# Kernel tuning notes

Measured on AMD Instinct MI355X. Metric: run time of the kernel, lower is better.

## Reference

```python
import jax, jax.numpy as jnp
import numpy as np

H = 16  # head_num


def setup_inputs() -> dict:
    key = jax.random.key(0)
    ks = jax.random.split(key, 16)
    B, N, D, DR = 4, 512, 1024, 128
    dk = D // H
    nrm = lambda i, shp, sc=1.0: jax.random.normal(ks[i], shp, jnp.float32) * sc
    inp = {
        "q": nrm(0, (B, N, D)),
        "k": nrm(1, (B, N, D)),
        "v": nrm(2, (B, N, D)),
        "r_k": nrm(3, (B, N, N, DR), 0.1),
        "r_v": nrm(4, (B, N, N, DR), 0.1),
        # learned params (Linear stored as [in, out] so y = x @ W + b)
        "Wq": nrm(5, (D, D), 1.0 / np.sqrt(D)), "bq": jnp.zeros((D,), jnp.float32),
        "Wk": nrm(6, (D, D), 1.0 / np.sqrt(D)), "bk": jnp.zeros((D,), jnp.float32),
        "Wv": nrm(7, (D, D), 1.0 / np.sqrt(D)), "bv": jnp.zeros((D,), jnp.float32),
        "Wrk": nrm(8, (DR, dk), 1.0 / np.sqrt(DR)), "brk": jnp.zeros((dk,), jnp.float32),
        "Wrv": nrm(9, (DR, dk), 1.0 / np.sqrt(DR)), "brv": jnp.zeros((dk,), jnp.float32),
        "Wo": nrm(10, (D, D), 1.0 / np.sqrt(D)), "bo": jnp.zeros((D,), jnp.float32),
    }
    return inp


def reference(q, k, v, r_k, r_v, Wq, bq, Wk, bk, Wv, bv, Wrk, brk, Wrv, brv, Wo, bo):
    B, N, D = q.shape
    dk = D // H
    scale = 1.0 / np.sqrt(dk).astype(np.float32)
    # relation projections ('concat' mode, rel_share=False): [B,N,N,d_rel] -> [B,N,N,d_k]
    rk = r_k @ Wrk + brk
    rv = r_v @ Wrv + brv

    def heads(x, W, b):  # [B,N,D] -> [B,H,N,dk]
        return (x @ W + b).reshape(B, N, H, dk).transpose(0, 2, 1, 3)

    qh = heads(q, Wq, bq)
    kh = heads(k, Wk, bk)
    vh = heads(v, Wv, bv)
    # score_1: standard scaled dot-product; score_2: relation bias per (query m, key n)
    score = jnp.einsum('bhmd,bhnd->bhmn', qh, kh) * scale \
          + jnp.einsum('bhmd,bmnd->bhmn', qh, rk)
    att = jax.nn.softmax(score, axis=-1)  # [B,H,N,N]
    # value_1: standard AV; value_2: relation-value combination
    val = jnp.einsum('bhmn,bhnd->bhmd', att, vh) \
        + jnp.einsum('bhmn,bmnd->bhmd', att, rv)
    out = val.transpose(0, 2, 1, 3).reshape(B, N, D) @ Wo + bo
    return out
```

## Files before the change

### kernel.cpp

```cpp
#include <hip/hip_runtime.h>
#include <hip/hip_bf16.h>
#include <hip/hip_fp16.h>
#include <stdint.h>


typedef __attribute__((ext_vector_type(4))) float f32x4;
typedef __attribute__((ext_vector_type(8))) short s16x8;

#define MFMA16(A, B, C) __builtin_amdgcn_mfma_f32_16x16x32_bf16(A, B, C, 0, 0, 0)

__device__ __forceinline__ uint16_t f2bf(float x) {
  uint32_t u = __float_as_uint(x);
  u += 0x7fffu + ((u >> 16) & 1u);
  return (uint16_t)(u >> 16);
}
__device__ __forceinline__ float bf2f(uint16_t u) {
  return __uint_as_float((uint32_t)u << 16);
}
__device__ __forceinline__ uint16_t f2h(float x) {
  __half h = __float2half_rn(x);
  return *reinterpret_cast<uint16_t*>(&h);
}
__device__ __forceinline__ float h2f(uint16_t u) {
  __half h = *reinterpret_cast<__half*>(&u);
  return __half2float(h);
}

__device__ __forceinline__ s16x8 pack8(float4 a, float4 b) {
  s16x8 r;
  r[0] = (short)f2bf(a.x); r[1] = (short)f2bf(a.y); r[2] = (short)f2bf(a.z); r[3] = (short)f2bf(a.w);
  r[4] = (short)f2bf(b.x); r[5] = (short)f2bf(b.y); r[6] = (short)f2bf(b.z); r[7] = (short)f2bf(b.w);
  return r;
}

__device__ __forceinline__ void gll16(const void* g, void* l) {
  __builtin_amdgcn_global_load_lds(
      (const __attribute__((address_space(1))) uint32_t*)(g),
      (__attribute__((address_space(3))) uint32_t*)(l), 16, 0, 0);
}

__global__ __launch_bounds__(256) void k_prep(
    const float* __restrict__ Wq, const float* __restrict__ Wk,
    const float* __restrict__ Wv, const float* __restrict__ Wo,
    const float* __restrict__ Wrk, const float* __restrict__ Wrv,
    uint16_t* __restrict__ WqT, uint16_t* __restrict__ WkT,
    uint16_t* __restrict__ WvT, uint16_t* __restrict__ WoT,
    uint16_t* __restrict__ WrkB, uint16_t* __restrict__ WrvT) {
  int z = blockIdx.y;
  int t = threadIdx.x;
  if (z == 4) {
    if (blockIdx.x == 0) {
      for (int i = t; i < 128 * 64; i += 256) WrkB[i] = f2bf(Wrk[i]);
      for (int i = t; i < 64 * 128; i += 256) {
        int d = i >> 7, r = i & 127;
        WrvT[i] = f2bf(Wrv[r * 64 + d]);
      }
    }
    return;
  }
  const float* W = (z == 0) ? Wq : (z == 1) ? Wk : (z == 2) ? Wv : Wo;
  uint16_t* O = (z == 0) ? WqT : (z == 1) ? WkT : (z == 2) ? WvT : WoT;
  int tk = (blockIdx.x >> 4) * 64;
  int tn = (blockIdx.x & 15) * 64;
  __shared__ float tile[64][65];
  {
    int kk = t >> 2, c0 = (t & 3) * 16;
    const float* src = W + (size_t)(tk + kk) * 1024 + tn + c0;
#pragma unroll
    for (int i = 0; i < 16; i += 4) {
      float4 v = *(const float4*)(src + i);
      tile[kk][c0 + i + 0] = v.x; tile[kk][c0 + i + 1] = v.y;
      tile[kk][c0 + i + 2] = v.z; tile[kk][c0 + i + 3] = v.w;
    }
  }
  __syncthreads();
  {
    int n_loc = t >> 2;
    int n = tn + n_loc;
#pragma unroll
    for (int cc = 0; cc < 2; ++cc) {
      int c = (t & 3) * 2 + cc;
      int csrc = c ^ (n & 7);
      s16x8 pk;
#pragma unroll
      for (int j = 0; j < 8; ++j) pk[j] = (short)f2bf(tile[csrc * 8 + j][n_loc]);
      *reinterpret_cast<s16x8*>(O + (size_t)n * 1024 + tk + c * 8) = pk;
    }
  }
}

__global__ __launch_bounds__(256) void k_projqkv(
    const float* __restrict__ Xq, const float* __restrict__ Xk,
    const float* __restrict__ Xv, const uint16_t* __restrict__ WTbase,
    const float* __restrict__ bq, const float* __restrict__ bk,
    const float* __restrict__ bv, uint16_t* __restrict__ outbase) {
  int mode = blockIdx.z;
  const float* X = (mode == 0) ? Xq : (mode == 1) ? Xk : Xv;
  const float* bias = (mode == 0) ? bq : (mode == 1) ? bk : bv;
  const uint16_t* WT = WTbase + (size_t)mode * (1u << 20);
  uint16_t* out = outbase + (size_t)mode * (2u << 20);

  __shared__ alignas(16) uint16_t As[128 * 64];
  __shared__ alignas(16) uint16_t Bs[128 * 64];
  int t = threadIdx.x, lane = t & 63, w = t >> 6, lr = lane & 15, lg = lane >> 4;
  int m0 = blockIdx.x * 128, n0 = blockIdx.y * 128;
  int wm = (w >> 1) * 64, wn = (w & 1) * 64;
  f32x4 acc[4][4];
#pragma unroll
  for (int i = 0; i < 4; ++i)
#pragma unroll
    for (int j = 0; j < 4; ++j) acc[i][j] = (f32x4){0.f, 0.f, 0.f, 0.f};
  int srow = t >> 1, sh = t & 1;
  for (int ko = 0; ko < 16; ++ko) {
    __syncthreads();
    {
#pragma unroll
      for (int i = 0; i < 4; ++i) {
        int u = i * 256 + t;
        int row = u >> 3, c2 = u & 7;
        gll16(WT + (size_t)(n0 + row) * 1024 + ko * 64 + c2 * 8, (char*)Bs + u * 16);
      }
      const float* src = X + (size_t)(m0 + srow) * 1024 + ko * 64 + sh * 32;
#pragma unroll
      for (int c = 0; c < 4; ++c) {
        float4 v0 = *(const float4*)(src + c * 8);
        float4 v1 = *(const float4*)(src + c * 8 + 4);
        s16x8 pk = pack8(v0, v1);
        *reinterpret_cast<s16x8*>((char*)As + srow * 128 +
                                  ((((sh * 4 + c) * 16)) ^ ((srow & 7) << 4))) = pk;
      }
    }
    __syncthreads();
#pragma unroll
    for (int kk = 0; kk < 2; ++kk) {
      s16x8 af[4], bf[4];
#pragma unroll
      for (int mt = 0; mt < 4; ++mt) {
        int row = wm + mt * 16 + lr;
        af[mt] = *(const s16x8*)((const char*)As + row * 128 +
                                 (((kk * 32 + lg * 8) * 2) ^ ((row & 7) << 4)));
      }
#pragma unroll
      for (int nt = 0; nt < 4; ++nt) {
        int row = wn + nt * 16 + lr;
        bf[nt] = *(const s16x8*)((const char*)Bs + row * 128 +
                                 (((kk * 32 + lg * 8) * 2) ^ ((row & 7) << 4)));
      }
#pragma unroll
      for (int mt = 0; mt < 4; ++mt)
#pragma unroll
        for (int nt = 0; nt < 4; ++nt)
          acc[mt][nt] = MFMA16(af[mt], bf[nt], acc[mt][nt]);
    }
  }
  float sc = (mode == 1) ? 0.125f : 1.0f;
#pragma unroll
  for (int mt = 0; mt < 4; ++mt) {
#pragma unroll
    for (int nt = 0; nt < 4; ++nt) {
      int col = n0 + wn + nt * 16 + lr;
      float bcol = bias[col];
      if (mode != 2) {
#pragma unroll
        for (int r = 0; r < 4; ++r) {
          int row = m0 + wm + mt * 16 + lg * 4 + r;
          out[(size_t)row * 1024 + col] = f2bf((acc[mt][nt][r] + bcol) * sc);
        }
      } else {
        int row0 = m0 + wm + mt * 16 + lg * 4;
        int b = row0 >> 9, n = row0 & 511;
        int h = col >> 6, d = col & 63;
        ushort4 pk;
        pk.x = f2bf(acc[mt][nt][0] + bcol);
        pk.y = f2bf(acc[mt][nt][1] + bcol);
        pk.z = f2bf(acc[mt][nt][2] + bcol);
        pk.w = f2bf(acc[mt][nt][3] + bcol);
        *reinterpret_cast<ushort4*>(out + ((size_t)(b * 16 + h) * 64 + d) * 512 + n) = pk;
      }
    }
  }
}

__global__ __launch_bounds__(256) void k_qt(
    const uint16_t* __restrict__ qh, const uint16_t* __restrict__ WrkB,
    uint16_t* __restrict__ qt) {
  int t = threadIdx.x, lane = t & 63, w = t >> 6, lr = lane & 15, lg = lane >> 4;
  int row0 = blockIdx.x * 64 + w * 16;
  f32x4 acc[8];
#pragma unroll
  for (int i = 0; i < 8; ++i) acc[i] = (f32x4){0.f, 0.f, 0.f, 0.f};
  s16x8 af[2];
#pragma unroll
  for (int kk = 0; kk < 2; ++kk)
    af[kk] = *(const s16x8*)(qh + (size_t)(row0 + lr) * 64 + kk * 32 + lg * 8);
#pragma unroll
  for (int rt = 0; rt < 8; ++rt) {
#pragma unroll
    for (int kk = 0; kk < 2; ++kk) {
      s16x8 bf = *(const s16x8*)(WrkB + (size_t)(rt * 16 + lr) * 64 + kk * 32 + lg * 8);
      acc[rt] = MFMA16(af[kk], bf, acc[rt]);
    }
  }
#pragma unroll
  for (int rt = 0; rt < 8; ++rt)
#pragma unroll
    for (int r = 0; r < 4; ++r)
      qt[(size_t)(row0 + lg * 4 + r) * 128 + rt * 16 + lr] = f2bf(acc[rt][r]);
}

__global__ __launch_bounds__(256) void k_score1(
    const uint16_t* __restrict__ qh, const uint16_t* __restrict__ kh,
    uint16_t* __restrict__ S1) {
  __shared__ alignas(16) uint16_t As[128 * 64];
  __shared__ alignas(16) uint16_t Bs[128 * 64];
  int t = threadIdx.x, lane = t & 63, w = t >> 6, lr = lane & 15, lg = lane >> 4;
  int mt = blockIdx.x >> 2, nt = blockIdx.x & 3, h = blockIdx.y, b = blockIdx.z;
  int m0 = mt * 128, n0 = nt * 128;
  const char* qg = (const char*)(qh + (size_t)(b * 512 + m0) * 1024 + h * 64);
  const char* kg = (const char*)(kh + (size_t)(b * 512 + n0) * 1024 + h * 64);
#pragma unroll
  for (int i = 0; i < 4; ++i) {
    int u = i * 256 + t;
    int row = u >> 3;
    int cs = (u & 7) ^ (row & 7);
    gll16(qg + (size_t)row * 2048 + cs * 16, (char*)As + u * 16);
    gll16(kg + (size_t)row * 2048 + cs * 16, (char*)Bs + u * 16);
  }
  __syncthreads();
  int wm = (w >> 1) * 64, wn = (w & 1) * 64;
  f32x4 acc[4][4];
#pragma unroll
  for (int i = 0; i < 4; ++i)
#pragma unroll
    for (int j = 0; j < 4; ++j) acc[i][j] = (f32x4){0.f, 0.f, 0.f, 0.f};
#pragma unroll
  for (int kk = 0; kk < 2; ++kk) {
    s16x8 af[4], bf[4];
#pragma unroll
    for (int mtt = 0; mtt < 4; ++mtt) {
      int row = wm + mtt * 16 + lr;
      af[mtt] = *(const s16x8*)((const char*)As + row * 128 +
                                (((kk * 4 + lg) ^ (row & 7)) * 16));
    }
#pragma unroll
    for (int ntt = 0; ntt < 4; ++ntt) {
      int row = wn + ntt * 16 + lr;
      bf[ntt] = *(const s16x8*)((const char*)Bs + row * 128 +
                                (((kk * 4 + lg) ^ (row & 7)) * 16));
    }
#pragma unroll
    for (int mtt = 0; mtt < 4; ++mtt)
#pragma unroll
      for (int ntt = 0; ntt < 4; ++ntt)
        acc[mtt][ntt] = MFMA16(bf[ntt], af[mtt], acc[mtt][ntt]);
  }
  int hsw = (h & 7) << 3;
#pragma unroll
  for (int mtt = 0; mtt < 4; ++mtt) {
#pragma unroll
    for (int ntt = 0; ntt < 4; ++ntt) {
      int m = b * 512 + m0 + wm + mtt * 16 + lr;
      int nsw = (n0 + wn + ntt * 16 + lg * 4) ^ hsw;
      ushort4 u4;
      u4.x = f2h(acc[mtt][ntt][0]); u4.y = f2h(acc[mtt][ntt][1]);
      u4.z = f2h(acc[mtt][ntt][2]); u4.w = f2h(acc[mtt][ntt][3]);
      *(ushort4*)(S1 + (size_t)m * 8192 + h * 512 + nsw) = u4;
    }
  }
}

#define RKSTEP(s)                                                              \
  {                                                                            \
    asm volatile("s_waitcnt vmcnt(%0)" :: "i"(((s) < 31) ? 2 : 0) : "memory"); \
    const char* bp_ = wpriv + ((s) & 1) * 2048 + lr * 128;                     \
    float4 v0_ = *(const float4*)(bp_ + (((lg * 2 + 0) ^ (lr & 7)) * 16));     \
    float4 v1_ = *(const float4*)(bp_ + (((lg * 2 + 1) ^ (lr & 7)) * 16));     \
    acc[(s) >> 2] = MFMA16(aqt[(s) & 3], pack8(v0_, v1_), acc[(s) >> 2]);      \
    if ((s) + 2 < 32) {                                                        \
      const int s2_ = (s) + 2;                                                 \
      const char* src_ = rkb + (size_t)((s2_ >> 2) * 64 + w * 16 + r_lo) * 512 \
                         + (s2_ & 3) * 128 + c16s * 16;                        \
      char* dst_ = wpriv + (s2_ & 1) * 2048 + lane * 16;                       \
      gll16(src_, dst_);                                                       \
      gll16(src_ + 8 * 512, dst_ + 1024);                                      \
    }                                                                          \
  }

#define RVI(c)                                                                 \
  { _Pragma("unroll")                                                          \
    for (int i_ = 0; i_ < 2; ++i_) {                                           \
      int u_ = i_ * 64 + lane;                                                 \
      gll16(rvb + (size_t)(((c) >> 1) * 32 + (u_ >> 2)) * 512 + w * 128 +      \
                ((c) & 1) * 64 + (u_ & 3) * 16,                                \
            wpriv + ((c) & 1) * 2048 + u_ * 16);                               \
    } }

#define RVC(c, accv)                                                           \
  {                                                                            \
    s16x8 a_ = *(const s16x8*)((const char*)att_lds + lr * 1024 +              \
        (((uint32_t)(((c) >> 1) * 64 + lg * 16)) ^ ((uint32_t)(lr & 7) << 4)));\
    const float* vb_ = (const float*)(wpriv + ((c) & 1) * 2048);               \
    s16x8 bf_;                                                                 \
    _Pragma("unroll")                                                          \
    for (int i = 0; i < 8; ++i) bf_[i] = (short)f2bf(vb_[(lg * 8 + i) * 16 + lr]); \
    accv = MFMA16(a_, bf_, accv);                                              \
  }

__global__ __launch_bounds__(256, 4) void k_s2v2(
    const uint16_t* __restrict__ qt, const float* __restrict__ rk,
    const float* __restrict__ rv, uint16_t* SATT,
    const uint16_t* __restrict__ WrvT, const float* __restrict__ brv,
    uint16_t* __restrict__ V2) {
  int bm = blockIdx.x;
  int t = threadIdx.x, lane = t & 63, w = t >> 6, lr = lane & 15, lg = lane >> 4;
  __shared__ alignas(16) char stream_lds[16384];
  __shared__ alignas(16) uint16_t att_lds[16 * 512];
  __shared__ alignas(16) uint16_t arv_lds[16 * 128];
  __shared__ float red[2][16][4];
  char* wpriv = stream_lds + w * 4096;
  const int r_lo = lane >> 3;
  const int c16s = (lane & 7) ^ r_lo;

  s16x8 aqt[4];
#pragma unroll
  for (int kk = 0; kk < 4; ++kk)
    aqt[kk] = *(const s16x8*)(qt + ((size_t)bm * 16 + lr) * 128 + kk * 32 + lg * 8);
  const char* s1g = (const char*)(SATT + (size_t)bm * 8192);
#pragma unroll
  for (int i = 0; i < 4; ++i)
    gll16(s1g + i * 4096 + t * 16, (char*)att_lds + i * 4096 + t * 16);
  asm volatile("s_waitcnt vmcnt(0)" ::: "memory");

  const char* rkb = (const char*)(rk + (size_t)bm * 65536);
#pragma unroll
  for (int s2 = 0; s2 < 2; ++s2) {
    const char* src_ = rkb + (size_t)(w * 16 + r_lo) * 512 + s2 * 128 + c16s * 16;
    char* dst_ = wpriv + s2 * 2048 + lane * 16;
    gll16(src_, dst_);
    gll16(src_ + 8 * 512, dst_ + 1024);
  }

  f32x4 acc[8];
#pragma unroll
  for (int j = 0; j < 8; ++j) acc[j] = (f32x4){0.f, 0.f, 0.f, 0.f};

  RKSTEP(0)  RKSTEP(1)  RKSTEP(2)  RKSTEP(3)  RKSTEP(4)  RKSTEP(5)  RKSTEP(6)  RKSTEP(7)
  RKSTEP(8)  RKSTEP(9)  RKSTEP(10) RKSTEP(11) RKSTEP(12) RKSTEP(13) RKSTEP(14) RKSTEP(15)
  RKSTEP(16) RKSTEP(17) RKSTEP(18) RKSTEP(19) RKSTEP(20) RKSTEP(21) RKSTEP(22) RKSTEP(23)
  RKSTEP(24) RKSTEP(25) RKSTEP(26) RKSTEP(27) RKSTEP(28) RKSTEP(29) RKSTEP(30) RKSTEP(31)

  const char* rvb = (const char*)(rv + (size_t)bm * 65536);
  RVI(0) RVI(1)
  __syncthreads();

#pragma unroll
  for (int idx = 0; idx < 8; ++idx) {
#pragma unroll
    for (int r = 0; r < 4; ++r) {
      int h = lg * 4 + r;
      int n = idx * 64 + w * 16 + lr;
      uint16_t s1v = *(const uint16_t*)((const char*)att_lds + h * 1024 +
                     (((uint32_t)n * 2) ^ ((uint32_t)(h & 7) << 4)));
      acc[idx][r] += h2f(s1v);
    }
  }

  float mrow[4], inv[4];
#pragma unroll
  for (int r = 0; r < 4; ++r) {
    float mx = acc[0][r];
#pragma unroll
    for (int j = 1; j < 8; ++j) mx = fmaxf(mx, acc[j][r]);
#pragma unroll
    for (int off = 1; off < 16; off <<= 1) mx = fmaxf(mx, __shfl_xor(mx, off, 64));
    mrow[r] = mx;
  }
  if (lr == 0) {
#pragma unroll
    for (int r = 0; r < 4; ++r) red[0][lg * 4 + r][w] = mrow[r];
  }
  __syncthreads();
#pragma unroll
  for (int r = 0; r < 4; ++r) {
    const float* p = red[0][lg * 4 + r];
    mrow[r] = fmaxf(fmaxf(p[0], p[1]), fmaxf(p[2], p[3]));
  }
#pragma unroll
  for (int r = 0; r < 4; ++r) {
    float s = 0.f;
#pragma unroll
    for (int j = 0; j < 8; ++j) {
      float pj = __expf(acc[j][r] - mrow[r]);
      acc[j][r] = pj;
      s += pj;
    }
#pragma unroll
    for (int off = 1; off < 16; off <<= 1) s += __shfl_xor(s, off, 64);
    inv[r] = s;
  }
  if (lr == 0) {
#pragma unroll
    for (int r = 0; r < 4; ++r) red[1][lg * 4 + r][w] = inv[r];
  }
  __syncthreads();
#pragma unroll
  for (int r = 0; r < 4; ++r) {
    const float* p = red[1][lg * 4 + r];
    inv[r] = 1.f / (p[0] + p[1] + p[2] + p[3]);
  }
#pragma unroll
  for (int r = 0; r < 4; ++r) {
    int h = lg * 4 + r;
#pragma unroll
    for (int idx = 0; idx < 8; ++idx) {
      int n = idx * 64 + w * 16 + lr;
      uint32_t off = (uint32_t)h * 1024 + (((uint32_t)n * 2) ^ ((uint32_t)(h & 7) << 4));
      *(uint16_t*)((char*)att_lds + off) = f2bf(acc[idx][r] * inv[r]);
    }
  }
  __syncthreads();

  f32x4 arv0 = (f32x4){0.f, 0.f, 0.f, 0.f}, arv1 = arv0;
#pragma unroll 1
  for (int cp = 0; cp < 14; ++cp) {
    asm volatile("s_waitcnt vmcnt(2)" ::: "memory");
    RVC(2 * cp, arv0)
    RVI(2 * cp + 2)
    asm volatile("s_waitcnt vmcnt(2)" ::: "memory");
    RVC(2 * cp + 1, arv1)
    RVI(2 * cp + 3)
  }
  asm volatile("s_waitcnt vmcnt(2)" ::: "memory");
  RVC(28, arv0)
  RVI(30)
  asm volatile("s_waitcnt vmcnt(2)" ::: "memory");
  RVC(29, arv1)
  RVI(31)
  asm volatile("s_waitcnt vmcnt(2)" ::: "memory");
  RVC(30, arv0)
  asm volatile("s_waitcnt vmcnt(0)" ::: "memory");
  RVC(31, arv1)

#pragma unroll
  for (int r = 0; r < 4; ++r) {
    int h = lg * 4 + r;
    uint32_t rc0 = (uint32_t)(w * 32 + lr) * 2;
    uint32_t rc1 = (uint32_t)(w * 32 + 16 + lr) * 2;
    *(uint16_t*)((char*)arv_lds + h * 256 + (rc0 ^ ((uint32_t)(h & 7) << 4))) = f2bf(arv0[r]);
    *(uint16_t*)((char*)arv_lds + h * 256 + (rc1 ^ ((uint32_t)(h & 7) << 4))) = f2bf(arv1[r]);
  }
  __syncthreads();
  f32x4 vacc = (f32x4){0.f, 0.f, 0.f, 0.f};
#pragma unroll
  for (int kk = 0; kk < 4; ++kk) {
    uint32_t rb = (uint32_t)(kk * 32 + lg * 8) * 2;
    s16x8 a = *(const s16x8*)((const char*)arv_lds + lr * 256 +
                              (rb ^ ((uint32_t)(lr & 7) << 4)));
    s16x8 bfw = *(const s16x8*)(WrvT + (size_t)(w * 16 + lr) * 128 + kk * 32 + lg * 8);
    vacc = MFMA16(a, bfw, vacc);
  }
  float bias = brv[w * 16 + lr];
#pragma unroll
  for (int r = 0; r < 4; ++r)
    V2[(size_t)bm * 1024 + (lg * 4 + r) * 64 + w * 16 + lr] = f2bf(vacc[r] + bias);

#pragma unroll
  for (int i = 0; i < 4; ++i) {
    s16x8 vv = *(const s16x8*)((const char*)att_lds + i * 4096 + t * 16);
    *(s16x8*)((char*)SATT + (size_t)bm * 16384 + i * 4096 + t * 16) = vv;
  }
}

__global__ __launch_bounds__(256) void k_val1(
    const uint16_t* __restrict__ vhT, const uint16_t* __restrict__ ATT,
    const uint16_t* __restrict__ V2, uint16_t* __restrict__ VALB) {
  int t = threadIdx.x, lane = t & 63, w = t >> 6, lr = lane & 15, lg = lane >> 4;
  int mt = blockIdx.x >> 1, dh = blockIdx.x & 1, h = blockIdx.y, b = blockIdx.z;
  int mb = mt * 64 + w * 16;
  const uint16_t* vrow = vhT + ((size_t)((b * 16 + h) * 64) + dh * 32 + lr) * 512 + lg * 8;
  const uint16_t* arow = ATT + (size_t)(b * 512 + mb + lr) * 8192 + h * 512;
  f32x4 acc[2];
#pragma unroll
  for (int j = 0; j < 2; ++j) acc[j] = (f32x4){0.f, 0.f, 0.f, 0.f};
#pragma unroll 4
  for (int kk = 0; kk < 16; ++kk) {
    int nsw = (kk * 32 + lg * 8) ^ ((h & 7) << 3);
    s16x8 a0 = *(const s16x8*)(arow + nsw);
#pragma unroll
    for (int dt = 0; dt < 2; ++dt) {
      s16x8 vf = *(const s16x8*)(vrow + (size_t)dt * 16 * 512 + kk * 32);
      acc[dt] = MFMA16(vf, a0, acc[dt]);
    }
  }
#pragma unroll
  for (int dt = 0; dt < 2; ++dt) {
    size_t adr = (size_t)(b * 512 + mb + lr) * 1024 + h * 64 + dh * 32 + dt * 16 + lg * 4;
    ushort4 v2v = *(const ushort4*)(V2 + adr);
    ushort4 o;
    o.x = f2bf(acc[dt][0] + bf2f(v2v.x));
    o.y = f2bf(acc[dt][1] + bf2f(v2v.y));
    o.z = f2bf(acc[dt][2] + bf2f(v2v.z));
    o.w = f2bf(acc[dt][3] + bf2f(v2v.w));
    *(ushort4*)(VALB + adr) = o;
  }
}

__global__ __launch_bounds__(256) void k_out(
    const uint16_t* __restrict__ A, const uint16_t* __restrict__ WT,
    const float* __restrict__ bias, float* __restrict__ out) {
  __shared__ alignas(16) uint16_t As[128 * 64];
  __shared__ alignas(16) uint16_t Bs[128 * 64];
  int t = threadIdx.x, lane = t & 63, w = t >> 6, lr = lane & 15, lg = lane >> 4;
  int m0 = blockIdx.x * 128, n0 = blockIdx.y * 128;
  int wm = (w >> 1) * 64, wn = (w & 1) * 64;
  f32x4 acc[4][4];
#pragma unroll
  for (int i = 0; i < 4; ++i)
#pragma unroll
    for (int j = 0; j < 4; ++j) acc[i][j] = (f32x4){0.f, 0.f, 0.f, 0.f};
  int srow = t >> 1, sh = t & 1;
  for (int ko = 0; ko < 16; ++ko) {
    __syncthreads();
    {
#pragma unroll
      for (int i = 0; i < 4; ++i) {
        int u = i * 256 + t;
        int row = u >> 3, c2 = u & 7;
        gll16(WT + (size_t)(n0 + row) * 1024 + ko * 64 + c2 * 8, (char*)Bs + u * 16);
      }
      const uint16_t* asrc = A + (size_t)(m0 + srow) * 1024 + ko * 64 + sh * 32;
#pragma unroll
      for (int c = 0; c < 4; ++c) {
        s16x8 va = *(const s16x8*)(asrc + c * 8);
        *reinterpret_cast<s16x8*>((char*)As + srow * 128 +
                                  ((((sh * 4 + c) * 16)) ^ ((srow & 7) << 4))) = va;
      }
    }
    __syncthreads();
#pragma unroll
    for (int kk = 0; kk < 2; ++kk) {
      s16x8 af[4], bf[4];
#pragma unroll
      for (int mt = 0; mt < 4; ++mt) {
        int row = wm + mt * 16 + lr;
        af[mt] = *(const s16x8*)((const char*)As + row * 128 +
                                 (((kk * 32 + lg * 8) * 2) ^ ((row & 7) << 4)));
      }
#pragma unroll
      for (int nt = 0; nt < 4; ++nt) {
        int row = wn + nt * 16 + lr;
        bf[nt] = *(const s16x8*)((const char*)Bs + row * 128 +
                                 (((kk * 32 + lg * 8) * 2) ^ ((row & 7) << 4)));
      }
#pragma unroll
      for (int mt = 0; mt < 4; ++mt)
#pragma unroll
        for (int nt = 0; nt < 4; ++nt)
          acc[mt][nt] = MFMA16(af[mt], bf[nt], acc[mt][nt]);
    }
  }
#pragma unroll
  for (int mt = 0; mt < 4; ++mt) {
#pragma unroll
    for (int nt = 0; nt < 4; ++nt) {
      int col = n0 + wn + nt * 16 + lr;
      float bcol = bias[col];
#pragma unroll
      for (int r = 0; r < 4; ++r) {
        int row = m0 + wm + mt * 16 + lg * 4 + r;
        out[(size_t)row * 1024 + col] = acc[mt][nt][r] + bcol;
      }
    }
  }
}

extern "C" void kernel_launch(void* const* d_in, const int* in_sizes, int n_in,
                              void* d_out, int out_size, void* d_ws, size_t ws_size,
                              hipStream_t stream) {
  const float* q   = (const float*)d_in[0];
  const float* k_  = (const float*)d_in[1];
  const float* v   = (const float*)d_in[2];
  const float* r_k = (const float*)d_in[3];
  const float* r_v = (const float*)d_in[4];
  const float* Wq  = (const float*)d_in[5];
  const float* bq  = (const float*)d_in[6];
  const float* Wk  = (const float*)d_in[7];
  const float* bk  = (const float*)d_in[8];
  const float* Wv  = (const float*)d_in[9];
  const float* bv  = (const float*)d_in[10];
  const float* Wrk = (const float*)d_in[11];
  const float* Wrv = (const float*)d_in[13];
  const float* brv = (const float*)d_in[14];
  const float* Wo  = (const float*)d_in[15];
  const float* bo  = (const float*)d_in[16];
  (void)in_sizes; (void)n_in; (void)out_size;

  char* ws = (char*)d_ws;
  uint16_t* WqT  = (uint16_t*)(ws + (size_t)(0));
  uint16_t* WkT  = (uint16_t*)(ws + (size_t)(2u << 20));
  uint16_t* WvT  = (uint16_t*)(ws + (size_t)(4u << 20));
  uint16_t* WoT  = (uint16_t*)(ws + (size_t)(6u << 20));
  uint16_t* WrkB = (uint16_t*)(ws + (size_t)(8u << 20));
  uint16_t* WrvT = (uint16_t*)(ws + (size_t)(8u << 20) + (64u << 10));
  uint16_t* QH   = (uint16_t*)(ws + (size_t)(16u << 20));
  uint16_t* KH   = (uint16_t*)(ws + (size_t)(20u << 20));
  uint16_t* VHT  = (uint16_t*)(ws + (size_t)(24u << 20));
  uint16_t* QT   = (uint16_t*)(ws + (size_t)(28u << 20));
  uint16_t* VALB = (uint16_t*)(ws + (size_t)(36u << 20));
  uint16_t* V2   = (uint16_t*)(ws + (size_t)(16u << 20));
  uint16_t* SATT = (uint16_t*)(ws + (size_t)(40u << 20));
  if (ws_size < (size_t)(74u << 20)) return;

  dim3 blk(256, 1, 1);
  k_prep<<<dim3(256, 5, 1), blk, 0, stream>>>(Wq, Wk, Wv, Wo, Wrk, Wrv,
                                              WqT, WkT, WvT, WoT, WrkB, WrvT);
  k_projqkv<<<dim3(16, 8, 3), blk, 0, stream>>>(q, k_, v, WqT, bq, bk, bv, QH);
  k_qt<<<dim3(512, 1, 1), blk, 0, stream>>>(QH, WrkB, QT);
  k_score1<<<dim3(16, 16, 4), blk, 0, stream>>>(QH, KH, SATT);
  k_s2v2<<<dim3(2048, 1, 1), blk, 0, stream>>>(QT, r_k, r_v, SATT, WrvT, brv, V2);
  k_val1<<<dim3(16, 16, 4), blk, 0, stream>>>(VHT, SATT, V2, VALB);
  k_out<<<dim3(16, 8, 1), blk, 0, stream>>>(VALB, WoT, bo, (float*)d_out);
}
```

Before: 382.4 us.

## Merge qt and score1 launches, use packed bf16 converts, overlap S1 load

Folds the small qt projection kernel into the score1 launch as extra blocks along the y grid dimension, removing one kernel launch and letting both run concurrently. Replaces scalar float-to-bf16 rounding with the hardware v_cvt_pk_bf16_f32 instruction in pack8 and the rv conversion path. In k_s2v2, the S1 attention-row load is issued after the first rk prefetches, with adjusted vmcnt waits, so it overlaps the rk stream instead of stalling up front. The barrier is moved before the rv loads. The packed convert may round slightly differently from the manual routine.

```diff
diff --git a/kernel.cpp b/kernel.cpp
--- a/kernel.cpp
+++ b/kernel.cpp
@@ -26,11 +26,19 @@
   return __half2float(h);
 }
 
+__device__ __forceinline__ uint32_t cvtpk(float lo, float hi) {
+  uint32_t r;
+  asm("v_cvt_pk_bf16_f32 %0, %1, %2" : "=v"(r) : "v"(lo), "v"(hi));
+  return r;
+}
+
 __device__ __forceinline__ s16x8 pack8(float4 a, float4 b) {
-  s16x8 r;
-  r[0] = (short)f2bf(a.x); r[1] = (short)f2bf(a.y); r[2] = (short)f2bf(a.z); r[3] = (short)f2bf(a.w);
-  r[4] = (short)f2bf(b.x); r[5] = (short)f2bf(b.y); r[6] = (short)f2bf(b.z); r[7] = (short)f2bf(b.w);
-  return r;
+  union { uint32_t u[4]; s16x8 v; } r;
+  r.u[0] = cvtpk(a.x, a.y);
+  r.u[1] = cvtpk(a.z, a.w);
+  r.u[2] = cvtpk(b.x, b.y);
+  r.u[3] = cvtpk(b.z, b.w);
+  return r.v;
 }
 
 __device__ __forceinline__ void gll16(const void* g, void* l) {
@@ -181,40 +189,43 @@
   }
 }
 
-__global__ __launch_bounds__(256) void k_qt(
-    const uint16_t* __restrict__ qh, const uint16_t* __restrict__ WrkB,
+__global__ __launch_bounds__(256) void k_score1qt(
+    const uint16_t* __restrict__ qh, const uint16_t* __restrict__ kh,
+    const uint16_t* __restrict__ WrkB, uint16_t* __restrict__ S1,
     uint16_t* __restrict__ qt) {
-  int t = threadIdx.x, lane = t & 63, w = t >> 6, lr = lane & 15, lg = lane >> 4;
-  int row0 = blockIdx.x * 64 + w * 16;
-  f32x4 acc[8];
-#pragma unroll
-  for (int i = 0; i < 8; ++i) acc[i] = (f32x4){0.f, 0.f, 0.f, 0.f};
-  s16x8 af[2];
-#pragma unroll
-  for (int kk = 0; kk < 2; ++kk)
-    af[kk] = *(const s16x8*)(qh + (size_t)(row0 + lr) * 64 + kk * 32 + lg * 8);
-#pragma unroll
-  for (int rt = 0; rt < 8; ++rt) {
-#pragma unroll
-    for (int kk = 0; kk < 2; ++kk) {
-      s16x8 bf = *(const s16x8*)(WrkB + (size_t)(rt * 16 + lr) * 64 + kk * 32 + lg * 8);
-      acc[rt] = MFMA16(af[kk], bf, acc[rt]);
-    }
-  }
-#pragma unroll
-  for (int rt = 0; rt < 8; ++rt)
-#pragma unroll
-    for (int r = 0; r < 4; ++r)
-      qt[(size_t)(row0 + lg * 4 + r) * 128 + rt * 16 + lr] = f2bf(acc[rt][r]);
-}
-
-__global__ __launch_bounds__(256) void k_score1(
-    const uint16_t* __restrict__ qh, const uint16_t* __restrict__ kh,
-    uint16_t* __restrict__ S1) {
   __shared__ alignas(16) uint16_t As[128 * 64];
   __shared__ alignas(16) uint16_t Bs[128 * 64];
   int t = threadIdx.x, lane = t & 63, w = t >> 6, lr = lane & 15, lg = lane >> 4;
-  int mt = blockIdx.x >> 2, nt = blockIdx.x & 3, h = blockIdx.y, b = blockIdx.z;
+  int b = blockIdx.z;
+  if (blockIdx.y >= 16) {
+    int slot = (blockIdx.y - 16) * 64 + b * 16 + blockIdx.x;
+#pragma unroll
+    for (int it = 0; it < 2; ++it) {
+      int row0 = slot * 128 + it * 64 + w * 16;
+      f32x4 acc[8];
+#pragma unroll
+      for (int i = 0; i < 8; ++i) acc[i] = (f32x4){0.f, 0.f, 0.f, 0.f};
+      s16x8 af[2];
+#pragma unroll
+      for (int kk = 0; kk < 2; ++kk)
+        af[kk] = *(const s16x8*)(qh + (size_t)(row0 + lr) * 64 + kk * 32 + lg * 8);
+#pragma unroll
+      for (int rt = 0; rt < 8; ++rt) {
+#pragma unroll
+        for (int kk = 0; kk < 2; ++kk) {
+          s16x8 bf = *(const s16x8*)(WrkB + (size_t)(rt * 16 + lr) * 64 + kk * 32 + lg * 8);
+          acc[rt] = MFMA16(af[kk], bf, acc[rt]);
+        }
+      }
+#pragma unroll
+      for (int rt = 0; rt < 8; ++rt)
+#pragma unroll
+        for (int r = 0; r < 4; ++r)
+          qt[(size_t)(row0 + lg * 4 + r) * 128 + rt * 16 + lr] = f2bf(acc[rt][r]);
+    }
+    return;
+  }
+  int mt = blockIdx.x >> 2, nt = blockIdx.x & 3, h = blockIdx.y;
   int m0 = mt * 128, n0 = nt * 128;
   const char* qg = (const char*)(qh + (size_t)(b * 512 + m0) * 1024 + h * 64);
   const char* kg = (const char*)(kh + (size_t)(b * 512 + n0) * 1024 + h * 64);
@@ -271,7 +282,8 @@
 
 #define RKSTEP(s)                                                              \
   {                                                                            \
-    asm volatile("s_waitcnt vmcnt(%0)" :: "i"(((s) < 31) ? 2 : 0) : "memory"); \
+    asm volatile("s_waitcnt vmcnt(%0)" ::                                      \
+                 "i"(((s) < 2) ? 6 : (((s) < 31) ? 2 : 0)) : "memory");        \
     const char* bp_ = wpriv + ((s) & 1) * 2048 + lr * 128;                     \
     float4 v0_ = *(const float4*)(bp_ + (((lg * 2 + 0) ^ (lr & 7)) * 16));     \
     float4 v1_ = *(const float4*)(bp_ + (((lg * 2 + 1) ^ (lr & 7)) * 16));     \
@@ -300,10 +312,12 @@
     s16x8 a_ = *(const s16x8*)((const char*)att_lds + lr * 1024 +              \
         (((uint32_t)(((c) >> 1) * 64 + lg * 16)) ^ ((uint32_t)(lr & 7) << 4)));\
     const float* vb_ = (const float*)(wpriv + ((c) & 1) * 2048);               \
-    s16x8 bf_;                                                                 \
+    union { uint32_t u[4]; s16x8 v; } bb_;                                     \
     _Pragma("unroll")                                                          \
-    for (int i = 0; i < 8; ++i) bf_[i] = (short)f2bf(vb_[(lg * 8 + i) * 16 + lr]); \
-    accv = MFMA16(a_, bf_, accv);                                              \
+    for (int i = 0; i < 4; ++i)                                                \
+      bb_.u[i] = cvtpk(vb_[(lg * 8 + 2 * i) * 16 + lr],                        \
+                       vb_[(lg * 8 + 2 * i + 1) * 16 + lr]);                   \
+    accv = MFMA16(a_, bb_.v, accv);                                            \
   }
 
 __global__ __launch_bounds__(256, 4) void k_s2v2(
@@ -325,11 +339,6 @@
 #pragma unroll
   for (int kk = 0; kk < 4; ++kk)
     aqt[kk] = *(const s16x8*)(qt + ((size_t)bm * 16 + lr) * 128 + kk * 32 + lg * 8);
-  const char* s1g = (const char*)(SATT + (size_t)bm * 8192);
-#pragma unroll
-  for (int i = 0; i < 4; ++i)
-    gll16(s1g + i * 4096 + t * 16, (char*)att_lds + i * 4096 + t * 16);
-  asm volatile("s_waitcnt vmcnt(0)" ::: "memory");
 
   const char* rkb = (const char*)(rk + (size_t)bm * 65536);
 #pragma unroll
@@ -339,6 +348,10 @@
     gll16(src_, dst_);
     gll16(src_ + 8 * 512, dst_ + 1024);
   }
+  const char* s1g = (const char*)(SATT + (size_t)bm * 8192);
+#pragma unroll
+  for (int i = 0; i < 4; ++i)
+    gll16(s1g + i * 4096 + t * 16, (char*)att_lds + i * 4096 + t * 16);
 
   f32x4 acc[8];
 #pragma unroll
@@ -349,9 +362,10 @@
   RKSTEP(16) RKSTEP(17) RKSTEP(18) RKSTEP(19) RKSTEP(20) RKSTEP(21) RKSTEP(22) RKSTEP(23)
   RKSTEP(24) RKSTEP(25) RKSTEP(26) RKSTEP(27) RKSTEP(28) RKSTEP(29) RKSTEP(30) RKSTEP(31)
 
+  __syncthreads();
+
   const char* rvb = (const char*)(rv + (size_t)bm * 65536);
   RVI(0) RVI(1)
-  __syncthreads();
 
 #pragma unroll
   for (int idx = 0; idx < 8; ++idx) {
@@ -615,8 +629,7 @@
   k_prep<<<dim3(256, 5, 1), blk, 0, stream>>>(Wq, Wk, Wv, Wo, Wrk, Wrv,
                                               WqT, WkT, WvT, WoT, WrkB, WrvT);
   k_projqkv<<<dim3(16, 8, 3), blk, 0, stream>>>(q, k_, v, WqT, bq, bk, bv, QH);
-  k_qt<<<dim3(512, 1, 1), blk, 0, stream>>>(QH, WrkB, QT);
-  k_score1<<<dim3(16, 16, 4), blk, 0, stream>>>(QH, KH, SATT);
+  k_score1qt<<<dim3(16, 20, 4), blk, 0, stream>>>(QH, KH, WrkB, SATT, QT);
   k_s2v2<<<dim3(2048, 1, 1), blk, 0, stream>>>(QT, r_k, r_v, SATT, WrvT, brv, V2);
   k_val1<<<dim3(16, 16, 4), blk, 0, stream>>>(VHT, SATT, V2, VALB);
   k_out<<<dim3(16, 8, 1), blk, 0, stream>>>(VALB, WoT, bo, (float*)d_out);
```

After: 372.3 us. 1.03x faster.
